# Kernel tuning notes

Hardware: AMD Instinct MI355X
Metric: run time of the kernel (lower is better)

## Reference

```python
import jax, jax.numpy as jnp
import numpy as np

STRIDE = 2
PAD = 1


def _deform_conv2d(x, offset, mask, weight, bias):
    # Modulated deformable conv2d (torchvision semantics), offset_groups=1,
    # stride=2, padding=1, dilation=1, groups=1.
    B, C, H, W = x.shape
    Cout, Cin, kH, kW = weight.shape
    K = kH * kW
    _, _, Ho, Wo = mask.shape

    off = offset.reshape(B, K, 2, Ho, Wo)  # [:, :, 0]=dy, [:, :, 1]=dx
    ii = jnp.repeat(jnp.arange(kH), kW).astype(x.dtype)  # [K] kernel row index
    jj = jnp.tile(jnp.arange(kW), kH).astype(x.dtype)    # [K] kernel col index
    gy = (jnp.arange(Ho) * STRIDE - PAD).astype(x.dtype)  # [Ho] base y of output pixel
    gx = (jnp.arange(Wo) * STRIDE - PAD).astype(x.dtype)  # [Wo] base x

    # Fractional sampling positions per (batch, kernel point, out pixel): [B,K,Ho,Wo]
    py = off[:, :, 0] + gy[None, None, :, None] + ii[None, :, None, None]
    px = off[:, :, 1] + gx[None, None, None, :] + jj[None, :, None, None]

    y0 = jnp.floor(py)
    x0 = jnp.floor(px)
    dy = py - y0
    dx = px - x0

    xf = x.reshape(B, C, H * W)

    def gather(yc, xc):
        # Bilinear corner gather with zero padding outside the image.
        valid = (yc >= 0) & (yc <= H - 1) & (xc >= 0) & (xc <= W - 1)
        yi = jnp.clip(yc, 0, H - 1).astype(jnp.int32)
        xi = jnp.clip(xc, 0, W - 1).astype(jnp.int32)
        idx = (yi * W + xi).reshape(B, 1, K * Ho * Wo)
        g = jnp.take_along_axis(xf, jnp.broadcast_to(idx, (B, C, K * Ho * Wo)), axis=2)
        return g.reshape(B, C, K, Ho, Wo) * valid[:, None].astype(x.dtype)

    w00 = ((1 - dy) * (1 - dx))[:, None]
    w01 = ((1 - dy) * dx)[:, None]
    w10 = (dy * (1 - dx))[:, None]
    w11 = (dy * dx)[:, None]

    val = (gather(y0, x0) * w00 + gather(y0, x0 + 1) * w01
           + gather(y0 + 1, x0) * w10 + gather(y0 + 1, x0 + 1) * w11)
    val = val * mask[:, None]  # modulation: [B,C,K,Ho,Wo] * [B,1,K,Ho,Wo]

    out = jnp.einsum('bckhw,ock->bohw', val, weight.reshape(Cout, Cin, K))
    return out + bias[None, :, None, None]


def setup_inputs() -> dict:
    key = jax.random.key(0)
    k1, k2, k3, k4, k5 = jax.random.split(key, 5)
    B, C, H, W = 8, 128, 128, 128
    Cout, kH, kW = 128, 3, 3
    Ho = (H + 2 * PAD - kH) // STRIDE + 1
    Wo = (W + 2 * PAD - kW) // STRIDE + 1
    x = jax.random.normal(k1, (B, C, H, W), dtype=jnp.float32)
    offset = jax.random.normal(k2, (B, 2 * kH * kW, Ho, Wo), dtype=jnp.float32)
    mask = jax.random.uniform(k3, (B, kH * kW, Ho, Wo), dtype=jnp.float32)
    weight = jax.random.normal(k4, (Cout, C, kH, kW), dtype=jnp.float32)
    bias = jax.random.normal(k5, (Cout,), dtype=jnp.float32)
    return {"x": x, "offset": offset, "mask": mask, "weight": weight, "bias": bias}


def reference(x, offset, mask, weight, bias):
    return _deform_conv2d(x, offset, mask, weight, bias)
```

## Files before the change

kernel.cpp:

```cpp
#include <hip/hip_runtime.h>
#include <hip/hip_bf16.h>

typedef __attribute__((ext_vector_type(8))) short short8;
typedef __attribute__((ext_vector_type(4))) short short4v;
typedef __attribute__((ext_vector_type(4))) float f32x4;
typedef __attribute__((ext_vector_type(4))) int int4v;
typedef unsigned long long u64;

#define HH 128
#define WW 128
#define CC 128
#define COUT 128
#define HO 64
#define WO 64
#define KK 9
#define PXB 64
#define NREC (KK * PXB)

__device__ __forceinline__ unsigned short bf16bits(float f) {
    union { float f; unsigned u; } u; u.f = f;
    unsigned r = u.u + 0x7fffu + ((u.u >> 16) & 1u);
    return (unsigned short)(r >> 16);
}
__device__ __forceinline__ float b2f(unsigned short h) {
    union { unsigned u; float f; } v; v.u = ((unsigned)h) << 16; return v.f;
}

__global__ __launch_bounds__(256, 4)
void prep_kernel(const float* __restrict__ x, unsigned short* __restrict__ xt,
                 const float* __restrict__ w, unsigned short* __restrict__ wp,
                 float* __restrict__ out) {
    const int blk = blockIdx.x;
    const int t = threadIdx.x;
    __shared__ unsigned short tile[128][132];

    if (blk < 1024) {
        const int b = blk >> 7;
        const int y = blk & 127;
        const float* src = x + (((size_t)b * CC) * HH + y) * WW;
#pragma unroll 8
        for (int c0 = 0; c0 < CC; c0 += 2) {
            int c = c0 + (t >> 7);
            int xx = t & 127;
            tile[xx][c] = bf16bits(src[(size_t)c * (HH * WW) + xx]);
        }
        __syncthreads();
        unsigned short* dst = xt + (((size_t)b * HH + y) * WW) * CC;
#pragma unroll
        for (int it = 0; it < 4; ++it) {
            int lin = it * 256 + t;
            int xx = lin >> 3;
            int cb = (lin & 7) * 16;
            const u64* lp = (const u64*)&tile[xx][cb];
            u64* op = (u64*)(dst + (size_t)xx * CC + cb);
            op[0] = lp[0]; op[1] = lp[1]; op[2] = lp[2]; op[3] = lp[3];
        }
    } else if (blk < 1600) {
        int i = (blk - 1024) * 256 + t;
        if (i < KK * COUT * CC) {
            int kp = i / (COUT * CC);
            int r = i - kp * (COUT * CC);
            int o = r >> 7;
            int c = r & 127;
            wp[i] = bf16bits(w[((size_t)o * CC + c) * KK + kp]);
        }
    } else {
        f32x4* o4 = (f32x4*)out;
        size_t idx = (size_t)(blk - 1600) * 256 + t;
#pragma unroll
        for (int k = 0; k < 16; ++k)
            o4[idx + (size_t)k * 65536] = (f32x4){0.f, 0.f, 0.f, 0.f};
    }
}

template <bool SPLIT>
__global__ __launch_bounds__(256, 4)
void dcn15_kernel(const unsigned short* __restrict__ xt, const float* __restrict__ offset,
                  const float* __restrict__ mask, const unsigned short* __restrict__ wprep,
                  const float* __restrict__ bias, float* __restrict__ out) {
    const int blk = blockIdx.x;
    const int b = blk & 7;
    const int ho = (blk >> 3) & 63;
    const int chalf = SPLIT ? (blk >> 9) : 0;
    const int t = threadIdx.x;
    const int lane = t & 63;
    const int wid = t >> 6;

    __shared__ int            s_cidx[NREC][4];
    __shared__ float          s_w[NREC][4];
    __shared__ unsigned short s_val[PXB][72];

    for (int e = t; e < NREC; e += 256) {
        int kp = e >> 6;
        int wo = e & 63;
        int ky = kp / 3, kx = kp - ky * 3;
        float dy = offset[(((size_t)b * 18 + 2 * kp    ) * HO + ho) * WO + wo];
        float dx = offset[(((size_t)b * 18 + 2 * kp + 1) * HO + ho) * WO + wo];
        float m  = mask  [(((size_t)b * 9  + kp        ) * HO + ho) * WO + wo];
        float py = dy + (float)(2 * ho - 1 + ky);
        float px = dx + (float)(2 * wo - 1 + kx);
        float fy0 = floorf(py), fx0 = floorf(px);
        float ay = py - fy0, ax = px - fx0;
        int y0 = (int)fy0, x0 = (int)fx0;
        int y1 = y0 + 1, x1 = x0 + 1;
        bool vy0 = (unsigned)y0 < HH, vy1 = (unsigned)y1 < HH;
        bool vx0 = (unsigned)x0 < WW, vx1 = (unsigned)x1 < WW;
        float w00 = (vy0 && vx0) ? (1.f - ay) * (1.f - ax) * m : 0.f;
        float w01 = (vy0 && vx1) ? (1.f - ay) * ax * m : 0.f;
        float w10 = (vy1 && vx0) ? ay * (1.f - ax) * m : 0.f;
        float w11 = (vy1 && vx1) ? ay * ax * m : 0.f;
        int cy0 = min(max(y0, 0), HH - 1), cy1 = min(max(y1, 0), HH - 1);
        int cx0 = min(max(x0, 0), WW - 1), cx1 = min(max(x1, 0), WW - 1);
        s_cidx[e][0] = (cy0 * WW + cx0) * CC;
        s_cidx[e][1] = (cy0 * WW + cx1) * CC;
        s_cidx[e][2] = (cy1 * WW + cx0) * CC;
        s_cidx[e][3] = (cy1 * WW + cx1) * CC;
        s_w[e][0] = w00; s_w[e][1] = w01; s_w[e][2] = w10; s_w[e][3] = w11;
    }

    f32x4 acc[2][4];
#pragma unroll
    for (int i = 0; i < 2; ++i)
#pragma unroll
        for (int j = 0; j < 4; ++j) acc[i][j] = (f32x4){0.f, 0.f, 0.f, 0.f};

    const int o_base = wid * 32;
    const int l16 = lane & 15;
    const int lhi = lane >> 4;

    const unsigned short* xtb = xt + (size_t)b * (HH * WW * CC);
    const int gpx = t >> 2;
    const int gcb = (t & 3) * 16;

    const int cbeg = SPLIT ? chalf * 64 : 0;
    const int cend = SPLIT ? cbeg + 64 : CC;

    for (int c0 = cbeg; c0 < cend; c0 += 64) {
        for (int kp = 0; kp < KK; ++kp) {
            __syncthreads();

            int rec = kp * PXB + gpx;
            int4v ci = *(const int4v*)&s_cidx[rec][0];
            f32x4 wq = *(const f32x4*)&s_w[rec][0];
            const unsigned short* bp = xtb + c0 + gcb;
            short8 h00a = *(const short8*)(bp + ci.x);
            short8 h00b = *(const short8*)(bp + ci.x + 8);
            short8 h01a = *(const short8*)(bp + ci.y);
            short8 h01b = *(const short8*)(bp + ci.y + 8);
            short8 h10a = *(const short8*)(bp + ci.z);
            short8 h10b = *(const short8*)(bp + ci.z + 8);
            short8 h11a = *(const short8*)(bp + ci.w);
            short8 h11b = *(const short8*)(bp + ci.w + 8);

            const unsigned short* wb = wprep + (size_t)kp * (COUT * CC) + c0 + lhi * 8;
            short8 afr[2][2];
#pragma unroll
            for (int mr = 0; mr < 2; ++mr)
#pragma unroll
                for (int kk = 0; kk < 2; ++kk)
                    afr[mr][kk] = *(const short8*)(wb + (size_t)(o_base + mr * 16 + l16) * CC + kk * 32);

            short8 v0, v1;
#pragma unroll
            for (int j = 0; j < 8; ++j) {
                float val = wq.x * b2f((unsigned short)h00a[j]) + wq.y * b2f((unsigned short)h01a[j])
                          + wq.z * b2f((unsigned short)h10a[j]) + wq.w * b2f((unsigned short)h11a[j]);
                v0[j] = (short)bf16bits(val);
            }
#pragma unroll
            for (int j = 0; j < 8; ++j) {
                float val = wq.x * b2f((unsigned short)h00b[j]) + wq.y * b2f((unsigned short)h01b[j])
                          + wq.z * b2f((unsigned short)h10b[j]) + wq.w * b2f((unsigned short)h11b[j]);
                v1[j] = (short)bf16bits(val);
            }
            *(short8*)&s_val[gpx][gcb] = v0;
            *(short8*)&s_val[gpx][gcb + 8] = v1;

            __syncthreads();

#pragma unroll
            for (int nr = 0; nr < 4; ++nr) {
                short8 bfr[2];
#pragma unroll
                for (int kk = 0; kk < 2; ++kk)
                    bfr[kk] = *(const short8*)&s_val[nr * 16 + l16][kk * 32 + lhi * 8];
#pragma unroll
                for (int mr = 0; mr < 2; ++mr)
#pragma unroll
                    for (int kk = 0; kk < 2; ++kk)
                        acc[mr][nr] = __builtin_amdgcn_mfma_f32_16x16x32_bf16(
                            afr[mr][kk], bfr[kk], acc[mr][nr], 0, 0, 0);
            }
        }
    }

    float* ob = out + ((size_t)b * COUT) * (HO * WO) + (size_t)ho * WO;
    if (SPLIT) {
#pragma unroll
        for (int mr = 0; mr < 2; ++mr) {
            int o_r = o_base + mr * 16 + lhi * 4;
#pragma unroll
            for (int r = 0; r < 4; ++r) {
                int o = o_r + r;
                float bs = (chalf == 0) ? bias[o] : 0.f;
#pragma unroll
                for (int nr = 0; nr < 4; ++nr) {
                    int wo = nr * 16 + l16;
                    atomicAdd(&ob[(size_t)o * (HO * WO) + wo], acc[mr][nr][r] + bs);
                }
            }
        }
    } else {
#pragma unroll
        for (int mr = 0; mr < 2; ++mr) {
            int o_r = o_base + mr * 16 + lhi * 4;
#pragma unroll
            for (int r = 0; r < 4; ++r) {
                int o = o_r + r;
                float bs = bias[o];
#pragma unroll
                for (int nr = 0; nr < 4; ++nr) {
                    int wo = nr * 16 + l16;
                    ob[(size_t)o * (HO * WO) + wo] = acc[mr][nr][r] + bs;
                }
            }
        }
    }
}

#define PXB6 32
#define NREC6 (KK * PXB6)
template <bool PREP>
__global__ __launch_bounds__(256, 4)
void dcn6_kernel(const float* __restrict__ x, const float* __restrict__ offset,
                 const float* __restrict__ mask, const float* __restrict__ weight,
                 const unsigned short* __restrict__ wprep,
                 const float* __restrict__ bias, float* __restrict__ out) {
    const int blk = blockIdx.x;
    const int b = blk & 7;
    const int rr = blk >> 3;
    const int ho = rr >> 1;
    const int px0 = (rr & 1) * PXB6;
    const int t = threadIdx.x;
    const int lane = t & 63;
    const int wid = t >> 6;

    __shared__ int            s_off[NREC6][2];
    __shared__ float          s_wq[NREC6][4];
    __shared__ unsigned short s_wt6[COUT][40];
    __shared__ unsigned short s_val6[PXB6][40];

    for (int e = t; e < NREC6; e += 256) {
        int kp = e >> 5;
        int wo = px0 + (e & 31);
        int ky = kp / 3, kx = kp - ky * 3;
        float dy = offset[(((size_t)b * 18 + 2 * kp    ) * HO + ho) * WO + wo];
        float dx = offset[(((size_t)b * 18 + 2 * kp + 1) * HO + ho) * WO + wo];
        float m  = mask  [(((size_t)b * 9  + kp        ) * HO + ho) * WO + wo];
        float py = dy + (float)(2 * ho - 1 + ky);
        float px = dx + (float)(2 * wo - 1 + kx);
        float fy0 = floorf(py), fx0 = floorf(px);
        float ay = py - fy0, ax = px - fx0;
        int y0 = (int)fy0, x0 = (int)fx0;
        int y1 = y0 + 1, x1 = x0 + 1;
        bool vy0 = (unsigned)y0 < HH, vy1 = (unsigned)y1 < HH;
        bool vx0 = (unsigned)x0 < WW, vx1 = (unsigned)x1 < WW;
        float w00 = (vy0 && vx0) ? (1.f - ay) * (1.f - ax) * m : 0.f;
        float w01 = (vy0 && vx1) ? (1.f - ay) * ax * m : 0.f;
        float w10 = (vy1 && vx0) ? ay * (1.f - ax) * m : 0.f;
        float w11 = (vy1 && vx1) ? ay * ax * m : 0.f;
        int bx = min(max(x0, 0), WW - 2);
        float wA0 = (x0 == bx     ? w00 : 0.f) + (x1 == bx     ? w01 : 0.f);
        float wB0 = (x0 == bx + 1 ? w00 : 0.f) + (x1 == bx + 1 ? w01 : 0.f);
        float wA1 = (x0 == bx     ? w10 : 0.f) + (x1 == bx     ? w11 : 0.f);
        float wB1 = (x0 == bx + 1 ? w10 : 0.f) + (x1 == bx + 1 ? w11 : 0.f);
        int cy0 = min(max(y0, 0), HH - 1), cy1 = min(max(y1, 0), HH - 1);
        s_off[e][0] = cy0 * WW + bx;
        s_off[e][1] = cy1 * WW + bx;
        s_wq[e][0] = wA0; s_wq[e][1] = wB0; s_wq[e][2] = wA1; s_wq[e][3] = wB1;
    }

    f32x4 acc[2][2];
#pragma unroll
    for (int i = 0; i < 2; ++i)
#pragma unroll
        for (int j = 0; j < 2; ++j) acc[i][j] = (f32x4){0.f, 0.f, 0.f, 0.f};

    const int o_base = wid * 32;
    const int l16 = lane & 15;
    const int lhi = lane >> 4;
    const float* xb = x + (size_t)b * CC * HH * WW;
    const int gpx = t & 31;
    const int gcg = t >> 5;

    for (int c0 = 0; c0 < CC; c0 += 32) {
        for (int kp = 0; kp < KK; ++kp) {
            __syncthreads();
            if (PREP) {
                const unsigned short* src =
                    wprep + ((size_t)kp * COUT + (t >> 1)) * CC + c0 + (t & 1) * 16;
                short8 w0 = *(const short8*)(src);
                short8 w1 = *(const short8*)(src + 8);
                *(short8*)&s_wt6[t >> 1][(t & 1) * 16] = w0;
                *(short8*)&s_wt6[t >> 1][(t & 1) * 16 + 8] = w1;
            } else {
                int o = t & 127;
                int clb = (t >> 7) * 16;
                const float* wp = weight + (size_t)o * (CC * KK) + (size_t)(c0 + clb) * KK + kp;
                short8 w0, w1;
#pragma unroll
                for (int j = 0; j < 8; ++j) w0[j] = (short)bf16bits(wp[j * KK]);
#pragma unroll
                for (int j = 0; j < 8; ++j) w1[j] = (short)bf16bits(wp[(8 + j) * KK]);
                *(short8*)&s_wt6[o][clb] = w0;
                *(short8*)&s_wt6[o][clb + 8] = w1;
            }
            {
                int rec = kp * PXB6 + gpx;
                int o0 = s_off[rec][0], o1 = s_off[rec][1];
                f32x4 wq = *(const f32x4*)&s_wq[rec][0];
                const float* pl = xb + (size_t)(c0 + gcg * 4) * (HH * WW);
                short4v v;
#pragma unroll
                for (int j = 0; j < 4; ++j) {
                    const float* p = pl + (size_t)j * (HH * WW);
                    float2 f0 = *(const float2*)(p + o0);
                    float2 f1 = *(const float2*)(p + o1);
                    float val = wq.x * f0.x + wq.y * f0.y + wq.z * f1.x + wq.w * f1.y;
                    v[j] = (short)bf16bits(val);
                }
                *(short4v*)&s_val6[gpx][gcg * 4] = v;
            }
            __syncthreads();
            short8 afr[2];
#pragma unroll
            for (int mr = 0; mr < 2; ++mr)
                afr[mr] = *(const short8*)&s_wt6[o_base + mr * 16 + l16][lhi * 8];
            short8 bfr[2];
#pragma unroll
            for (int nr = 0; nr < 2; ++nr)
                bfr[nr] = *(const short8*)&s_val6[nr * 16 + l16][lhi * 8];
#pragma unroll
            for (int mr = 0; mr < 2; ++mr)
#pragma unroll
                for (int nr = 0; nr < 2; ++nr)
                    acc[mr][nr] = __builtin_amdgcn_mfma_f32_16x16x32_bf16(
                        afr[mr], bfr[nr], acc[mr][nr], 0, 0, 0);
        }
    }

    float* ob = out + ((size_t)b * COUT) * (HO * WO) + (size_t)ho * WO;
#pragma unroll
    for (int mr = 0; mr < 2; ++mr) {
        int o_r = o_base + mr * 16 + lhi * 4;
#pragma unroll
        for (int r = 0; r < 4; ++r) {
            int o = o_r + r;
            float bs = bias[o];
#pragma unroll
            for (int nr = 0; nr < 2; ++nr) {
                int wo = px0 + nr * 16 + l16;
                ob[(size_t)o * (HO * WO) + wo] = acc[mr][nr][r] + bs;
            }
        }
    }
}

extern "C" void kernel_launch(void* const* d_in, const int* in_sizes, int n_in,
                              void* d_out, int out_size, void* d_ws, size_t ws_size,
                              hipStream_t stream) {
    (void)in_sizes; (void)n_in; (void)out_size;
    const float* x      = (const float*)d_in[0];
    const float* offset = (const float*)d_in[1];
    const float* mask   = (const float*)d_in[2];
    const float* weight = (const float*)d_in[3];
    const float* bias   = (const float*)d_in[4];
    float* out = (float*)d_out;

    const size_t wbytes  = (size_t)KK * COUT * CC * sizeof(unsigned short);
    const size_t xtoff   = (size_t)1 << 20;
    const size_t xtbytes = (size_t)8 * HH * WW * CC * sizeof(unsigned short);

    if (ws_size >= xtoff + xtbytes) {
        unsigned short* wp  = (unsigned short*)d_ws;
        unsigned short* xtp = (unsigned short*)((char*)d_ws + xtoff);
        prep_kernel<<<dim3(1856), dim3(256), 0, stream>>>(x, xtp, weight, wp, out);
        dcn15_kernel<true><<<dim3(1024), dim3(256), 0, stream>>>(xtp, offset, mask, wp, bias, out);
    } else if (ws_size >= wbytes) {
        unsigned short* wp = (unsigned short*)d_ws;
        dcn6_kernel<false><<<dim3(1024), dim3(256), 0, stream>>>(x, offset, mask, weight, nullptr, bias, out);
    } else {
        dcn6_kernel<false><<<dim3(1024), dim3(256), 0, stream>>>(x, offset, mask, weight, nullptr, bias, out);
    }
}
```

Baseline: 69.68 us.

## Replace atomic split-K reduction with partial buffer and last-block fixup

```diff
diff --git a/kernel.cpp b/kernel.cpp
--- a/kernel.cpp
+++ b/kernel.cpp
@@ -29,7 +29,7 @@
 __global__ __launch_bounds__(256, 4)
 void prep_kernel(const float* __restrict__ x, unsigned short* __restrict__ xt,
                  const float* __restrict__ w, unsigned short* __restrict__ wp,
-                 float* __restrict__ out) {
+                 int* __restrict__ cnt) {
     const int blk = blockIdx.x;
     const int t = threadIdx.x;
     __shared__ unsigned short tile[128][132];
@@ -65,19 +65,17 @@
             wp[i] = bf16bits(w[((size_t)o * CC + c) * KK + kp]);
         }
     } else {
-        f32x4* o4 = (f32x4*)out;
-        size_t idx = (size_t)(blk - 1600) * 256 + t;
-#pragma unroll
-        for (int k = 0; k < 16; ++k)
-            o4[idx + (size_t)k * 65536] = (f32x4){0.f, 0.f, 0.f, 0.f};
+        cnt[t] = 0;
+        cnt[t + 256] = 0;
     }
 }
 
 template <bool SPLIT>
 __global__ __launch_bounds__(256, 4)
-void dcn15_kernel(const unsigned short* __restrict__ xt, const float* __restrict__ offset,
+void dcn16_kernel(const unsigned short* __restrict__ xt, const float* __restrict__ offset,
                   const float* __restrict__ mask, const unsigned short* __restrict__ wprep,
-                  const float* __restrict__ bias, float* __restrict__ out) {
+                  const float* __restrict__ bias, float* __restrict__ out,
+                  float* __restrict__ part1, int* __restrict__ cnt) {
     const int blk = blockIdx.x;
     const int b = blk & 7;
     const int ho = (blk >> 3) & 63;
@@ -89,6 +87,7 @@
     __shared__ int            s_cidx[NREC][4];
     __shared__ float          s_w[NREC][4];
     __shared__ unsigned short s_val[PXB][72];
+    __shared__ int            s_last;
 
     for (int e = t; e < NREC; e += 256) {
         int kp = e >> 6;
@@ -195,22 +194,7 @@
     }
 
     float* ob = out + ((size_t)b * COUT) * (HO * WO) + (size_t)ho * WO;
-    if (SPLIT) {
-#pragma unroll
-        for (int mr = 0; mr < 2; ++mr) {
-            int o_r = o_base + mr * 16 + lhi * 4;
-#pragma unroll
-            for (int r = 0; r < 4; ++r) {
-                int o = o_r + r;
-                float bs = (chalf == 0) ? bias[o] : 0.f;
-#pragma unroll
-                for (int nr = 0; nr < 4; ++nr) {
-                    int wo = nr * 16 + l16;
-                    atomicAdd(&ob[(size_t)o * (HO * WO) + wo], acc[mr][nr][r] + bs);
-                }
-            }
-        }
-    } else {
+    if (!SPLIT) {
 #pragma unroll
         for (int mr = 0; mr < 2; ++mr) {
             int o_r = o_base + mr * 16 + lhi * 4;
@@ -223,6 +207,75 @@
                     int wo = nr * 16 + l16;
                     ob[(size_t)o * (HO * WO) + wo] = acc[mr][nr][r] + bs;
                 }
+            }
+        }
+        return;
+    }
+
+    const int pair = blk & 511;
+    if (chalf == 1) {
+        float* pb = part1 + (size_t)pair * 8192;
+#pragma unroll
+        for (int mr = 0; mr < 2; ++mr)
+#pragma unroll
+            for (int nr = 0; nr < 4; ++nr)
+                *(f32x4*)&pb[(size_t)(mr * 4 + nr) * 1024 + t * 4] = acc[mr][nr];
+    } else {
+#pragma unroll
+        for (int mr = 0; mr < 2; ++mr) {
+            int o_r = o_base + mr * 16 + lhi * 4;
+#pragma unroll
+            for (int r = 0; r < 4; ++r) {
+                int o = o_r + r;
+#pragma unroll
+                for (int nr = 0; nr < 4; ++nr) {
+                    int wo = nr * 16 + l16;
+                    ob[(size_t)o * (HO * WO) + wo] = acc[mr][nr][r];
+                }
+            }
+        }
+    }
+    __threadfence();
+    if (t == 0) s_last = atomicAdd(&cnt[pair], 1);
+    __syncthreads();
+    if (s_last != 1) return;
+
+    __threadfence();
+    if (chalf == 0) {
+        const float* pb = part1 + (size_t)pair * 8192;
+#pragma unroll
+        for (int mr = 0; mr < 2; ++mr)
+#pragma unroll
+            for (int nr = 0; nr < 4; ++nr) {
+                f32x4 p = *(const f32x4*)&pb[(size_t)(mr * 4 + nr) * 1024 + t * 4];
+                acc[mr][nr] = p + acc[mr][nr];
+            }
+    } else {
+#pragma unroll
+        for (int mr = 0; mr < 2; ++mr) {
+            int o_r = o_base + mr * 16 + lhi * 4;
+#pragma unroll
+            for (int r = 0; r < 4; ++r) {
+                int o = o_r + r;
+#pragma unroll
+                for (int nr = 0; nr < 4; ++nr) {
+                    int wo = nr * 16 + l16;
+                    acc[mr][nr][r] = ob[(size_t)o * (HO * WO) + wo] + acc[mr][nr][r];
+                }
+            }
+        }
+    }
+#pragma unroll
+    for (int mr = 0; mr < 2; ++mr) {
+        int o_r = o_base + mr * 16 + lhi * 4;
+#pragma unroll
+        for (int r = 0; r < 4; ++r) {
+            int o = o_r + r;
+            float bs = bias[o];
+#pragma unroll
+            for (int nr = 0; nr < 4; ++nr) {
+                int wo = nr * 16 + l16;
+                ob[(size_t)o * (HO * WO) + wo] = acc[mr][nr][r] + bs;
             }
         }
     }
@@ -378,17 +431,25 @@
     float* out = (float*)d_out;
 
     const size_t wbytes  = (size_t)KK * COUT * CC * sizeof(unsigned short);
+    const size_t cntoff  = (size_t)512 << 10;
     const size_t xtoff   = (size_t)1 << 20;
     const size_t xtbytes = (size_t)8 * HH * WW * CC * sizeof(unsigned short);
-
-    if (ws_size >= xtoff + xtbytes) {
+    const size_t p1off   = xtoff + xtbytes;
+    const size_t p1bytes = (size_t)512 * 8192 * sizeof(float);
+
+    if (ws_size >= p1off + p1bytes) {
         unsigned short* wp  = (unsigned short*)d_ws;
+        int* cnt            = (int*)((char*)d_ws + cntoff);
         unsigned short* xtp = (unsigned short*)((char*)d_ws + xtoff);
-        prep_kernel<<<dim3(1856), dim3(256), 0, stream>>>(x, xtp, weight, wp, out);
-        dcn15_kernel<true><<<dim3(1024), dim3(256), 0, stream>>>(xtp, offset, mask, wp, bias, out);
-    } else if (ws_size >= wbytes) {
-        unsigned short* wp = (unsigned short*)d_ws;
-        dcn6_kernel<false><<<dim3(1024), dim3(256), 0, stream>>>(x, offset, mask, weight, nullptr, bias, out);
+        float* p1           = (float*)((char*)d_ws + p1off);
+        prep_kernel<<<dim3(1601), dim3(256), 0, stream>>>(x, xtp, weight, wp, cnt);
+        dcn16_kernel<true><<<dim3(1024), dim3(256), 0, stream>>>(xtp, offset, mask, wp, bias, out, p1, cnt);
+    } else if (ws_size >= p1off) {
+        unsigned short* wp  = (unsigned short*)d_ws;
+        int* cnt            = (int*)((char*)d_ws + cntoff);
+        unsigned short* xtp = (unsigned short*)((char*)d_ws + xtoff);
+        prep_kernel<<<dim3(1601), dim3(256), 0, stream>>>(x, xtp, weight, wp, cnt);
+        dcn16_kernel<false><<<dim3(512), dim3(256), 0, stream>>>(xtp, offset, mask, wp, bias, out, nullptr, cnt);
     } else {
         dcn6_kernel<false><<<dim3(1024), dim3(256), 0, stream>>>(x, offset, mask, weight, nullptr, bias, out);
     }
```

Measured after the change: 236.4 us. +239.2%, slower.
